# Kernel optimization log

Measured on AMD Instinct MI355X. Metric: run time of the kernel, lower is better.

Reference implementation:

```python
import jax, jax.numpy as jnp
import numpy as np

N, N1, N2, K = 65536, 16384, 8192, 16
INDIM, HID, OUT = 64, 32, 128


def _knn_np(pos, q, k, chunk=1024):
    # brute-force chunked KNN (indices into pos) for setup only
    out = []
    for s in range(0, q.shape[0], chunk):
        d = ((q[s:s + chunk, None, :] - pos[None, :, :]) ** 2).sum(-1)
        out.append(np.argpartition(d, k, axis=1)[:, :k])
    return np.concatenate(out, 0)


def setup_inputs() -> dict:
    key = jax.random.key(0)
    ks = jax.random.split(key, 12)
    x = jax.random.normal(ks[0], (N, INDIM), jnp.float32)
    pos = jax.random.uniform(ks[1], (N, 3), jnp.float32)

    pos_np = np.asarray(pos)
    rng = np.random.default_rng(0)
    idx1 = np.sort(rng.choice(N, N1, replace=False))            # RandomSampler(ratio1)
    nn1 = _knn_np(pos_np, pos_np[idx1], K)                      # [N1, K] into full cloud
    src1, dst1 = nn1.reshape(-1), np.repeat(np.arange(N1), K)
    pos1 = pos_np[idx1]
    idx2 = np.sort(rng.choice(N1, N2, replace=False))           # RandomSampler(ratio2)
    nn2 = _knn_np(pos1, pos1[idx2], K)                          # [N2, K] into level-1 cloud
    src2, dst2 = nn2.reshape(-1), np.repeat(np.arange(N2), K)

    def lin(k, i, o):
        return jax.random.normal(k, (i, o), jnp.float32) / float(np.sqrt(i))

    return dict(
        x=x, pos=pos,
        W_down=lin(ks[2], INDIM, HID), b_down=jnp.zeros((HID,), jnp.float32),
        W_pp1=lin(ks[3], 10, 32), b_pp1=jnp.zeros((32,), jnp.float32),
        W_att1=lin(ks[4], 64, 64), b_att1=jnp.zeros((64,), jnp.float32),
        W_g1=lin(ks[5], 64, 64), b_g1=jnp.zeros((64,), jnp.float32),
        W_pp2=lin(ks[6], 10, 64), b_pp2=jnp.zeros((64,), jnp.float32),
        W_att2=lin(ks[7], 128, 128), b_att2=jnp.zeros((128,), jnp.float32),
        W_g2=lin(ks[8], 128, 128), b_g2=jnp.zeros((128,), jnp.float32),
        W_up=lin(ks[9], 128, OUT), b_up=jnp.zeros((OUT,), jnp.float32),
        W_sc=lin(ks[10], INDIM, OUT), b_sc=jnp.zeros((OUT,), jnp.float32),
        idx1=jnp.asarray(idx1, jnp.int32), idx2=jnp.asarray(idx2, jnp.int32),
        src1=jnp.asarray(src1, jnp.int32), dst1=jnp.asarray(dst1, jnp.int32),
        src2=jnp.asarray(src2, jnp.int32), dst2=jnp.asarray(dst2, jnp.int32),
    )


def _mlp(h, W, b):
    return jax.nn.relu(h @ W + b)


def _randla_conv(x, pos_all, pos_q, src, dst, Wpp, bpp, Watt, batt, Wg, bg, n_out):
    # RandlaKernel.message + add-aggregate + update (bipartite: targets = sampled points)
    pos_i, pos_j = pos_q[dst], pos_all[src]                     # [E,3]
    vij = pos_i - pos_j
    dij = jnp.sqrt((vij * vij).sum(-1, keepdims=True))          # [E,1]
    rel = jnp.concatenate([pos_i, pos_j, vij, dij], axis=1)     # [E,10]
    rij = _mlp(rel, Wpp, bpp)                                   # point_pos_nn
    fij = jnp.concatenate([x[src], rij], axis=1)                # [E, c+d]
    s = jax.nn.softmax(_mlp(fij, Watt, batt), axis=-1)          # softmax over feature dim (as in source)
    agg = jax.ops.segment_sum(s * fij, dst, num_segments=n_out) # aggr='add'
    return _mlp(agg, Wg, bg)                                    # global_nn


def reference(x, pos, W_down, b_down, W_pp1, b_pp1, W_att1, b_att1, W_g1, b_g1,
              W_pp2, b_pp2, W_att2, b_att2, W_g2, b_g2, W_up, b_up, W_sc, b_sc,
              idx1, idx2, src1, dst1, src2, dst2):
    h = _mlp(x, W_down, b_down)                                 # features_downsample (indim -> outdim//4)
    pos1 = pos[idx1]
    h = _randla_conv(h, pos, pos1, src1, dst1, W_pp1, b_pp1, W_att1, b_att1, W_g1, b_g1, N1)
    pos2 = pos1[idx2]
    h = _randla_conv(h, pos1, pos2, src2, dst2, W_pp2, b_pp2, W_att2, b_att2, W_g2, b_g2, N2)
    h = _mlp(h, W_up, b_up)                                     # features_upsample
    sc = _mlp(x[idx1][idx2], W_sc, b_sc)                        # shortcut resized, idx = idx1[idx2]
    return jax.nn.relu(h + sc)
```

## Files before the change

### kernel.cpp

```cpp
#include <hip/hip_runtime.h>

#define N_FULL 65536
#define NN1    16384
#define NN2    8192

typedef __attribute__((ext_vector_type(8))) short bf16x8;
typedef __attribute__((ext_vector_type(4))) float f32x4;
typedef unsigned short ushortT;

#define MFMA16(acc, a, b) acc = __builtin_amdgcn_mfma_f32_16x16x32_bf16(a, b, acc, 0, 0, 0)

#if __has_builtin(__builtin_amdgcn_cvt_pk_bf16_f32)
typedef __attribute__((ext_vector_type(2))) __bf16 bf16x2t;
static __device__ __forceinline__ unsigned pack2(float a, float b) {
    union { bf16x2t v; unsigned u; } c;
    c.v = __builtin_amdgcn_cvt_pk_bf16_f32(a, b);
    return c.u;
}
static __device__ __forceinline__ ushortT f2bf(float f) {
    union { bf16x2t v; ushortT s[2]; } c;
    c.v = __builtin_amdgcn_cvt_pk_bf16_f32(f, 0.f);
    return c.s[0];
}
#else
static __device__ __forceinline__ ushortT f2bf(float f) {
    union { float f; unsigned u; } v; v.f = f;
    unsigned r = v.u + 0x7FFFu + ((v.u >> 16) & 1u);
    return (ushortT)(r >> 16);
}
static __device__ __forceinline__ unsigned pack2(float a, float b) {
    return (unsigned)f2bf(a) | ((unsigned)f2bf(b) << 16);
}
#endif

static __device__ __forceinline__ float bfu2f(ushortT h) {
    union { unsigned u; float f; } v; v.u = (unsigned)h << 16; return v.f;
}

#define WS_WAT1  2304
#define WS_WGT1  6912
#define WS_WAT2  11520
#define WS_WGT2  28928
#define WS_WUPT  46336
#define WS_WSCT  63744
#define WS_H0    73728
#define WS_H1    (WS_H0 + 65536u*32u)

#define SMAX_SHIFT 24.0f

static __device__ __forceinline__ void tpose(
    const float* __restrict__ src, ushortT* __restrict__ dst,
    int K, int N, int STR, int gid, int gs)
{
    for (int i = gid; i < K * N; i += gs) {
        const int n = i / K, k = i - n * K;
        dst[n * STR + k] = f2bf(src[(size_t)k * N + n]);
    }
}

__global__ __launch_bounds__(256) void k_down(
    const float* __restrict__ x, const float* __restrict__ Wd,
    const float* __restrict__ bd,
    const float* __restrict__ Wa1, const float* __restrict__ Wg1,
    const float* __restrict__ Wa2, const float* __restrict__ Wg2,
    const float* __restrict__ Wup, const float* __restrict__ Wsc,
    ushortT* __restrict__ wsw, ushortT* __restrict__ h0w)
{
    const int t = threadIdx.x;
    if (blockIdx.x >= 512) {
        const int gid = (blockIdx.x - 512) * 256 + t, gs = 68 * 256;
        tpose(Wa1, wsw + WS_WAT1, 64, 64, 72, gid, gs);
        tpose(Wg1, wsw + WS_WGT1, 64, 64, 72, gid, gs);
        tpose(Wa2, wsw + WS_WAT2, 128, 128, 136, gid, gs);
        tpose(Wg2, wsw + WS_WGT2, 128, 128, 136, gid, gs);
        tpose(Wup, wsw + WS_WUPT, 128, 128, 136, gid, gs);
        tpose(Wsc, wsw + WS_WSCT, 64, 128, 72, gid, gs);
        return;
    }

    __shared__ __align__(16) ushortT Al[128 * 72];
    __shared__ __align__(16) ushortT Bl[32 * 72];
    const int rowBase = blockIdx.x * 128;

    {
        const int r = t >> 1, c0 = (t & 1) * 32;
        unsigned* dst = (unsigned*)Al + r * 36 + (c0 >> 1);
        const float* src = &x[(size_t)(rowBase + r) * 64 + c0];
#pragma unroll
        for (int j = 0; j < 32; j += 4) {
            const float4 v = *reinterpret_cast<const float4*>(src + j);
            dst[(j >> 1) + 0] = pack2(v.x, v.y);
            dst[(j >> 1) + 1] = pack2(v.z, v.w);
        }
        const int n = t >> 3, kc = (t & 7) * 8;
        float v[8];
#pragma unroll
        for (int j = 0; j < 8; ++j) v[j] = Wd[(size_t)(kc + j) * 32 + n];
        uint4 p;
        p.x = pack2(v[0], v[1]); p.y = pack2(v[2], v[3]);
        p.z = pack2(v[4], v[5]); p.w = pack2(v[6], v[7]);
        *(uint4*)((unsigned*)Bl + n * 36 + (kc >> 1)) = p;
    }
    __syncthreads();

    const int lane = t & 63, w = t >> 6, quad = lane >> 4, c16 = lane & 15;
    f32x4 acc[2][2];
#pragma unroll
    for (int mt = 0; mt < 2; ++mt)
#pragma unroll
        for (int nt = 0; nt < 2; ++nt)
#pragma unroll
            for (int r = 0; r < 4; ++r) acc[mt][nt][r] = 0.f;
#pragma unroll
    for (int ks = 0; ks < 2; ++ks) {
        bf16x8 a[2], b[2];
#pragma unroll
        for (int mt = 0; mt < 2; ++mt)
            a[mt] = *(const bf16x8*)&Al[(w * 32 + mt * 16 + c16) * 72 + ks * 32 + quad * 8];
#pragma unroll
        for (int nt = 0; nt < 2; ++nt)
            b[nt] = *(const bf16x8*)&Bl[(nt * 16 + c16) * 72 + ks * 32 + quad * 8];
#pragma unroll
        for (int mt = 0; mt < 2; ++mt)
#pragma unroll
            for (int nt = 0; nt < 2; ++nt) MFMA16(acc[mt][nt], a[mt], b[nt]);
    }
#pragma unroll
    for (int nt = 0; nt < 2; ++nt) {
        const int col = nt * 16 + c16;
        const float bias = bd[col];
#pragma unroll
        for (int mt = 0; mt < 2; ++mt)
#pragma unroll
            for (int r = 0; r < 4; ++r) {
                const int row = rowBase + w * 32 + mt * 16 + quad * 4 + r;
                h0w[(size_t)row * 32 + col] = f2bf(fmaxf(acc[mt][nt][r] + bias, 0.f));
            }
    }
}

__global__ __launch_bounds__(256) void k_conv1(
    const ushortT* __restrict__ h0w, const float* __restrict__ pos,
    const int* __restrict__ idx1, const int* __restrict__ src1,
    const float* __restrict__ Wpp, const float* __restrict__ bpp,
    const ushortT* __restrict__ wsw, const float* __restrict__ batt,
    const float* __restrict__ bg, ushortT* __restrict__ h1w)
{
    __shared__ __align__(16) ushortT Fl[64 * 72];
    __shared__ __align__(16) ushortT A2ls[16 * 72];
    __shared__ float Pl[352];
    const int t = threadIdx.x;
    const int d0 = blockIdx.x * 4;

    for (int i = t; i < 352; i += 256) Pl[i] = (i < 320) ? Wpp[i] : bpp[i - 320];
    for (int i = t; i < 432; i += 256) ((unsigned*)A2ls)[144 + i] = 0;

    {
        const int e = t >> 2, q = t & 3;
        const int g = e >> 4;
        const int s = src1[(d0 + g) * 16 + (e & 15)];
        ((uint4*)((unsigned*)Fl + e * 36))[q] =
            ((const uint4*)((const unsigned*)h0w + (size_t)s * 16))[q];

        const int pin = idx1[d0 + g];
        const float pix = pos[pin * 3 + 0], piy = pos[pin * 3 + 1], piz = pos[pin * 3 + 2];
        const float pjx = pos[s * 3 + 0],  pjy = pos[s * 3 + 1],  pjz = pos[s * 3 + 2];
        const float vx = pix - pjx, vy = piy - pjy, vz = piz - pjz;
        const float dij = sqrtf(vx * vx + vy * vy + vz * vz);
        const float rel[10] = {pix, piy, piz, pjx, pjy, pjz, vx, vy, vz, dij};
        __syncthreads();
        const int c0 = q * 8;
#pragma unroll
        for (int c = 0; c < 8; c += 2) {
            float a0 = Pl[320 + c0 + c], a1 = Pl[320 + c0 + c + 1];
#pragma unroll
            for (int i = 0; i < 10; ++i) {
                a0 += rel[i] * Pl[i * 32 + c0 + c];
                a1 += rel[i] * Pl[i * 32 + c0 + c + 1];
            }
            ((unsigned*)Fl)[(e * 72 + 32 + c0 + c) >> 1] = pack2(fmaxf(a0, 0.f), fmaxf(a1, 0.f));
        }
    }
    __syncthreads();

    const int lane = t & 63, w = t >> 6, quad = lane >> 4, c16 = lane & 15;
    const ushortT* WB = wsw + WS_WAT1;
    f32x4 acc[4];
#pragma unroll
    for (int nt = 0; nt < 4; ++nt)
#pragma unroll
        for (int r = 0; r < 4; ++r) acc[nt][r] = 0.f;
#pragma unroll
    for (int ks = 0; ks < 2; ++ks) {
        const bf16x8 a = *(const bf16x8*)&Fl[(w * 16 + c16) * 72 + ks * 32 + quad * 8];
#pragma unroll
        for (int nt = 0; nt < 4; ++nt) {
            const bf16x8 b = *(const bf16x8*)&WB[(nt * 16 + c16) * 72 + ks * 32 + quad * 8];
            MFMA16(acc[nt], a, b);
        }
    }
    float bcol[4];
#pragma unroll
    for (int nt = 0; nt < 4; ++nt) bcol[nt] = batt[nt * 16 + c16];

    float rs[4];
#pragma unroll
    for (int r = 0; r < 4; ++r) {
        float sm = 0.f;
#pragma unroll
        for (int nt = 0; nt < 4; ++nt) {
            const float a = fmaxf(acc[nt][r] + bcol[nt], 0.f);
            acc[nt][r] = __expf(a - SMAX_SHIFT);
            sm += acc[nt][r];
        }
        sm += __shfl_xor(sm, 1);
        sm += __shfl_xor(sm, 2);
        sm += __shfl_xor(sm, 4);
        sm += __shfl_xor(sm, 8);
        rs[r] = 1.f / sm;
    }
#pragma unroll
    for (int nt = 0; nt < 4; ++nt) {
        float v = 0.f;
#pragma unroll
        for (int r = 0; r < 4; ++r) {
            const float fv = bfu2f(Fl[(w * 16 + quad * 4 + r) * 72 + nt * 16 + c16]);
            v += acc[nt][r] * rs[r] * fv;
        }
        v += __shfl_xor(v, 16);
        v += __shfl_xor(v, 32);
        if (lane < 16)
            A2ls[w * 72 + nt * 16 + c16] = f2bf(v);
    }
    __syncthreads();

    {
        const ushortT* GB = wsw + WS_WGT1;
        f32x4 acc2 = {0.f, 0.f, 0.f, 0.f};
#pragma unroll
        for (int ks = 0; ks < 2; ++ks) {
            const bf16x8 a = *(const bf16x8*)&A2ls[c16 * 72 + ks * 32 + quad * 8];
            const bf16x8 b = *(const bf16x8*)&GB[(w * 16 + c16) * 72 + ks * 32 + quad * 8];
            MFMA16(acc2, a, b);
        }
        const int col = w * 16 + c16;
        const float bias = bg[col];
        if (quad == 0) {
#pragma unroll
            for (int r = 0; r < 4; ++r)
                h1w[(size_t)(d0 + r) * 64 + col] = f2bf(fmaxf(acc2[r] + bias, 0.f));
        }
    }
}

__global__ __launch_bounds__(256) void k_conv2f(
    const ushortT* __restrict__ h1w, const float* __restrict__ pos,
    const float* __restrict__ x,
    const int* __restrict__ idx1, const int* __restrict__ idx2,
    const int* __restrict__ src2,
    const float* __restrict__ Wpp, const float* __restrict__ bpp,
    const ushortT* __restrict__ wsw, const float* __restrict__ batt,
    const float* __restrict__ bg, const float* __restrict__ bup,
    const float* __restrict__ bsc, float* __restrict__ out)
{
    __shared__ __align__(16) ushortT Fl[64 * 136];
    __shared__ __align__(16) ushortT AGG[16 * 136];
    __shared__ __align__(16) ushortT H2[16 * 136];
    __shared__ float Pl[704];
    const int t = threadIdx.x;
    const int d0 = blockIdx.x * 4;

    for (int i = t; i < 704; i += 256) Pl[i] = (i < 640) ? Wpp[i] : bpp[i - 640];
    for (int i = t; i < 816; i += 256) ((unsigned*)AGG)[272 + i] = 0;

    {
        const int e = t >> 2, q = t & 3;
        const int g = e >> 4;
        const int s = src2[(d0 + g) * 16 + (e & 15)];
        {
            const uint4* srcp = (const uint4*)((const unsigned*)h1w + (size_t)s * 32);
            uint4* dstp = (uint4*)((unsigned*)Fl + e * 68);
            dstp[q * 2 + 0] = srcp[q * 2 + 0];
            dstp[q * 2 + 1] = srcp[q * 2 + 1];
        }
        const int pin = idx1[idx2[d0 + g]];
        const int sn = idx1[s];
        const float pix = pos[pin * 3 + 0], piy = pos[pin * 3 + 1], piz = pos[pin * 3 + 2];
        const float pjx = pos[sn * 3 + 0],  pjy = pos[sn * 3 + 1],  pjz = pos[sn * 3 + 2];
        const float vx = pix - pjx, vy = piy - pjy, vz = piz - pjz;
        const float dij = sqrtf(vx * vx + vy * vy + vz * vz);
        const float rel[10] = {pix, piy, piz, pjx, pjy, pjz, vx, vy, vz, dij};
        __syncthreads();
        const int c0 = q * 16;
#pragma unroll
        for (int c = 0; c < 16; c += 2) {
            float a0 = Pl[640 + c0 + c], a1 = Pl[640 + c0 + c + 1];
#pragma unroll
            for (int i = 0; i < 10; ++i) {
                a0 += rel[i] * Pl[i * 64 + c0 + c];
                a1 += rel[i] * Pl[i * 64 + c0 + c + 1];
            }
            ((unsigned*)Fl)[(e * 136 + 64 + c0 + c) >> 1] = pack2(fmaxf(a0, 0.f), fmaxf(a1, 0.f));
        }
    }
    __syncthreads();

    const int lane = t & 63, w = t >> 6, quad = lane >> 4, c16 = lane & 15;
    const ushortT* WB = wsw + WS_WAT2;
    f32x4 acc[8];
#pragma unroll
    for (int nt = 0; nt < 8; ++nt)
#pragma unroll
        for (int r = 0; r < 4; ++r) acc[nt][r] = 0.f;
#pragma unroll
    for (int ks = 0; ks < 4; ++ks) {
        const bf16x8 a = *(const bf16x8*)&Fl[(w * 16 + c16) * 136 + ks * 32 + quad * 8];
#pragma unroll
        for (int nt = 0; nt < 8; ++nt) {
            const bf16x8 b = *(const bf16x8*)&WB[(nt * 16 + c16) * 136 + ks * 32 + quad * 8];
            MFMA16(acc[nt], a, b);
        }
    }
    float bcol[8];
#pragma unroll
    for (int nt = 0; nt < 8; ++nt) bcol[nt] = batt[nt * 16 + c16];

    float rs[4];
#pragma unroll
    for (int r = 0; r < 4; ++r) {
        float sm = 0.f;
#pragma unroll
        for (int nt = 0; nt < 8; ++nt) {
            const float a = fmaxf(acc[nt][r] + bcol[nt], 0.f);
            acc[nt][r] = __expf(a - SMAX_SHIFT);
            sm += acc[nt][r];
        }
        sm += __shfl_xor(sm, 1);
        sm += __shfl_xor(sm, 2);
        sm += __shfl_xor(sm, 4);
        sm += __shfl_xor(sm, 8);
        rs[r] = 1.f / sm;
    }
#pragma unroll
    for (int nt = 0; nt < 8; ++nt) {
        float v = 0.f;
#pragma unroll
        for (int r = 0; r < 4; ++r) {
            const float fv = bfu2f(Fl[(w * 16 + quad * 4 + r) * 136 + nt * 16 + c16]);
            v += acc[nt][r] * rs[r] * fv;
        }
        v += __shfl_xor(v, 16);
        v += __shfl_xor(v, 32);
        if (lane < 16)
            AGG[w * 136 + nt * 16 + c16] = f2bf(v);
    }
    __syncthreads();


    {
        const ushortT* GB = wsw + WS_WGT2;
        f32x4 g[2];
#pragma unroll
        for (int j = 0; j < 2; ++j)
#pragma unroll
            for (int r = 0; r < 4; ++r) g[j][r] = 0.f;
#pragma unroll
        for (int ks = 0; ks < 4; ++ks) {
            const bf16x8 a = *(const bf16x8*)&AGG[c16 * 136 + ks * 32 + quad * 8];
#pragma unroll
            for (int j = 0; j < 2; ++j) {
                const bf16x8 b = *(const bf16x8*)&GB[((w * 2 + j) * 16 + c16) * 136 + ks * 32 + quad * 8];
                MFMA16(g[j], a, b);
            }
        }
#pragma unroll
        for (int j = 0; j < 2; ++j) {
            const int col = (w * 2 + j) * 16 + c16;
            const float bias = bg[col];
#pragma unroll
            for (int r = 0; r < 4; ++r)
                H2[(quad * 4 + r) * 136 + col] = f2bf(fmaxf(g[j][r] + bias, 0.f));
        }
    }
    __syncthreads();

    f32x4 u[2];
    {
        const ushortT* UB = wsw + WS_WUPT;
#pragma unroll
        for (int j = 0; j < 2; ++j)
#pragma unroll
            for (int r = 0; r < 4; ++r) u[j][r] = 0.f;
#pragma unroll
        for (int ks = 0; ks < 4; ++ks) {
            const bf16x8 a = *(const bf16x8*)&H2[c16 * 136 + ks * 32 + quad * 8];
#pragma unroll
            for (int j = 0; j < 2; ++j) {
                const bf16x8 b = *(const bf16x8*)&UB[((w * 2 + j) * 16 + c16) * 136 + ks * 32 + quad * 8];
                MFMA16(u[j], a, b);
            }
        }
#pragma unroll
        for (int j = 0; j < 2; ++j) {
            const float bias = bup[(w * 2 + j) * 16 + c16];
#pragma unroll
            for (int r = 0; r < 4; ++r) u[j][r] = fmaxf(u[j][r] + bias, 0.f);
        }
    }

    {
        const ushortT* SB = wsw + WS_WSCT;
        const int pinx = idx1[idx2[d0 + (c16 & 3)]];
        const float* xrow = &x[(size_t)pinx * 64];
        f32x4 s[2];
#pragma unroll
        for (int j = 0; j < 2; ++j)
#pragma unroll
            for (int r = 0; r < 4; ++r) s[j][r] = 0.f;
#pragma unroll
        for (int ks = 0; ks < 2; ++ks) {
            const float4 v0 = *reinterpret_cast<const float4*>(xrow + ks * 32 + quad * 8);
            const float4 v1 = *reinterpret_cast<const float4*>(xrow + ks * 32 + quad * 8 + 4);
            union { bf16x8 v; unsigned u[4]; } a;
            a.u[0] = pack2(v0.x, v0.y); a.u[1] = pack2(v0.z, v0.w);
            a.u[2] = pack2(v1.x, v1.y); a.u[3] = pack2(v1.z, v1.w);
#pragma unroll
            for (int j = 0; j < 2; ++j) {
                const bf16x8 b = *(const bf16x8*)&SB[((w * 2 + j) * 16 + c16) * 72 + ks * 32 + quad * 8];
                MFMA16(s[j], a.v, b);
            }
        }
        if (quad == 0) {
#pragma unroll
            for (int j = 0; j < 2; ++j) {
                const int col = (w * 2 + j) * 16 + c16;
                const float bias = bsc[col];
#pragma unroll
                for (int r = 0; r < 4; ++r) {
                    const float sc = fmaxf(s[j][r] + bias, 0.f);
                    out[(size_t)(d0 + r) * 128 + col] = u[j][r] + sc;
                }
            }
        }
    }
}

extern "C" void kernel_launch(void* const* d_in, const int* in_sizes, int n_in,
                              void* d_out, int out_size, void* d_ws, size_t ws_size,
                              hipStream_t stream)
{
    const float* x      = (const float*)d_in[0];
    const float* pos    = (const float*)d_in[1];
    const float* W_down = (const float*)d_in[2];
    const float* b_down = (const float*)d_in[3];
    const float* W_pp1  = (const float*)d_in[4];
    const float* b_pp1  = (const float*)d_in[5];
    const float* W_att1 = (const float*)d_in[6];
    const float* b_att1 = (const float*)d_in[7];
    const float* W_g1   = (const float*)d_in[8];
    const float* b_g1   = (const float*)d_in[9];
    const float* W_pp2  = (const float*)d_in[10];
    const float* b_pp2  = (const float*)d_in[11];
    const float* W_att2 = (const float*)d_in[12];
    const float* b_att2 = (const float*)d_in[13];
    const float* W_g2   = (const float*)d_in[14];
    const float* b_g2   = (const float*)d_in[15];
    const float* W_up   = (const float*)d_in[16];
    const float* b_up   = (const float*)d_in[17];
    const float* W_sc   = (const float*)d_in[18];
    const float* b_sc   = (const float*)d_in[19];
    const int* idx1 = (const int*)d_in[20];
    const int* idx2 = (const int*)d_in[21];
    const int* src1 = (const int*)d_in[22];
    const int* src2 = (const int*)d_in[24];

    ushortT* wsw = (ushortT*)d_ws;
    ushortT* h0w = wsw + WS_H0;
    ushortT* h1w = wsw + WS_H1;

    k_down  <<<512 + 68, 256, 0, stream>>>(x, W_down, b_down,
                                           W_att1, W_g1, W_att2, W_g2, W_up, W_sc,
                                           wsw, h0w);
    k_conv1 <<<NN1 / 4, 256, 0, stream>>>(h0w, pos, idx1, src1,
                                          W_pp1, b_pp1, wsw, b_att1, b_g1, h1w);
    k_conv2f<<<NN2 / 4, 256, 0, stream>>>(h1w, pos, x, idx1, idx2, src2,
                                          W_pp2, b_pp2, wsw, b_att2,
                                          b_g2, b_up, b_sc, (float*)d_out);
}
```

Before: 180.4 us.

## Process eight destination points per block to fill MFMA rows in conv kernels

New measurement: 170.9 us (median of 2 runs). 1.06x faster.

```diff
diff --git a/kernel.cpp b/kernel.cpp
--- a/kernel.cpp
+++ b/kernel.cpp
@@ -139,21 +139,21 @@
     }
 }
 
-__global__ __launch_bounds__(256) void k_conv1(
+__global__ __launch_bounds__(512) void k_conv1(
     const ushortT* __restrict__ h0w, const float* __restrict__ pos,
     const int* __restrict__ idx1, const int* __restrict__ src1,
     const float* __restrict__ Wpp, const float* __restrict__ bpp,
     const ushortT* __restrict__ wsw, const float* __restrict__ batt,
     const float* __restrict__ bg, ushortT* __restrict__ h1w)
 {
-    __shared__ __align__(16) ushortT Fl[64 * 72];
+    __shared__ __align__(16) ushortT Fl[128 * 72];
     __shared__ __align__(16) ushortT A2ls[16 * 72];
     __shared__ float Pl[352];
     const int t = threadIdx.x;
-    const int d0 = blockIdx.x * 4;
-
-    for (int i = t; i < 352; i += 256) Pl[i] = (i < 320) ? Wpp[i] : bpp[i - 320];
-    for (int i = t; i < 432; i += 256) ((unsigned*)A2ls)[144 + i] = 0;
+    const int d0 = blockIdx.x * 8;
+
+    for (int i = t; i < 352; i += 512) Pl[i] = (i < 320) ? Wpp[i] : bpp[i - 320];
+    for (int i = t; i < 288; i += 512) ((unsigned*)A2ls)[288 + i] = 0;
 
     {
         const int e = t >> 2, q = t & 3;
@@ -234,7 +234,7 @@
     }
     __syncthreads();
 
-    {
+    if (w < 4) {
         const ushortT* GB = wsw + WS_WGT1;
         f32x4 acc2 = {0.f, 0.f, 0.f, 0.f};
 #pragma unroll
@@ -245,15 +245,17 @@
         }
         const int col = w * 16 + c16;
         const float bias = bg[col];
-        if (quad == 0) {
-#pragma unroll
-            for (int r = 0; r < 4; ++r)
-                h1w[(size_t)(d0 + r) * 64 + col] = f2bf(fmaxf(acc2[r] + bias, 0.f));
-        }
-    }
-}
-
-__global__ __launch_bounds__(256) void k_conv2f(
+        if (quad < 2) {
+#pragma unroll
+            for (int r = 0; r < 4; ++r) {
+                const int row = quad * 4 + r;
+                h1w[(size_t)(d0 + row) * 64 + col] = f2bf(fmaxf(acc2[r] + bias, 0.f));
+            }
+        }
+    }
+}
+
+__global__ __launch_bounds__(512) void k_conv2f(
     const ushortT* __restrict__ h1w, const float* __restrict__ pos,
     const float* __restrict__ x,
     const int* __restrict__ idx1, const int* __restrict__ idx2,
@@ -263,15 +265,15 @@
     const float* __restrict__ bg, const float* __restrict__ bup,
     const float* __restrict__ bsc, float* __restrict__ out)
 {
-    __shared__ __align__(16) ushortT Fl[64 * 136];
+    __shared__ __align__(16) ushortT Fl[128 * 136];
     __shared__ __align__(16) ushortT AGG[16 * 136];
     __shared__ __align__(16) ushortT H2[16 * 136];
     __shared__ float Pl[704];
     const int t = threadIdx.x;
-    const int d0 = blockIdx.x * 4;
-
-    for (int i = t; i < 704; i += 256) Pl[i] = (i < 640) ? Wpp[i] : bpp[i - 640];
-    for (int i = t; i < 816; i += 256) ((unsigned*)AGG)[272 + i] = 0;
+    const int d0 = blockIdx.x * 8;
+
+    for (int i = t; i < 704; i += 512) Pl[i] = (i < 640) ? Wpp[i] : bpp[i - 640];
+    for (int i = t; i < 544; i += 512) ((unsigned*)AGG)[544 + i] = 0;
 
     {
         const int e = t >> 2, q = t & 3;
@@ -359,64 +361,40 @@
 
     {
         const ushortT* GB = wsw + WS_WGT2;
-        f32x4 g[2];
-#pragma unroll
-        for (int j = 0; j < 2; ++j)
-#pragma unroll
-            for (int r = 0; r < 4; ++r) g[j][r] = 0.f;
+        f32x4 g = {0.f, 0.f, 0.f, 0.f};
 #pragma unroll
         for (int ks = 0; ks < 4; ++ks) {
             const bf16x8 a = *(const bf16x8*)&AGG[c16 * 136 + ks * 32 + quad * 8];
-#pragma unroll
-            for (int j = 0; j < 2; ++j) {
-                const bf16x8 b = *(const bf16x8*)&GB[((w * 2 + j) * 16 + c16) * 136 + ks * 32 + quad * 8];
-                MFMA16(g[j], a, b);
-            }
-        }
-#pragma unroll
-        for (int j = 0; j < 2; ++j) {
-            const int col = (w * 2 + j) * 16 + c16;
-            const float bias = bg[col];
-#pragma unroll
-            for (int r = 0; r < 4; ++r)
-                H2[(quad * 4 + r) * 136 + col] = f2bf(fmaxf(g[j][r] + bias, 0.f));
-        }
-    }
-    __syncthreads();
-
-    f32x4 u[2];
+            const bf16x8 b = *(const bf16x8*)&GB[(w * 16 + c16) * 136 + ks * 32 + quad * 8];
+            MFMA16(g, a, b);
+        }
+        const int col = w * 16 + c16;
+        const float bias = bg[col];
+#pragma unroll
+        for (int r = 0; r < 4; ++r)
+            H2[(quad * 4 + r) * 136 + col] = f2bf(fmaxf(g[r] + bias, 0.f));
+    }
+    __syncthreads();
+
+    f32x4 u = {0.f, 0.f, 0.f, 0.f};
     {
         const ushortT* UB = wsw + WS_WUPT;
-#pragma unroll
-        for (int j = 0; j < 2; ++j)
-#pragma unroll
-            for (int r = 0; r < 4; ++r) u[j][r] = 0.f;
 #pragma unroll
         for (int ks = 0; ks < 4; ++ks) {
             const bf16x8 a = *(const bf16x8*)&H2[c16 * 136 + ks * 32 + quad * 8];
-#pragma unroll
-            for (int j = 0; j < 2; ++j) {
-                const bf16x8 b = *(const bf16x8*)&UB[((w * 2 + j) * 16 + c16) * 136 + ks * 32 + quad * 8];
-                MFMA16(u[j], a, b);
-            }
-        }
-#pragma unroll
-        for (int j = 0; j < 2; ++j) {
-            const float bias = bup[(w * 2 + j) * 16 + c16];
-#pragma unroll
-            for (int r = 0; r < 4; ++r) u[j][r] = fmaxf(u[j][r] + bias, 0.f);
-        }
+            const bf16x8 b = *(const bf16x8*)&UB[(w * 16 + c16) * 136 + ks * 32 + quad * 8];
+            MFMA16(u, a, b);
+        }
+        const float bias = bup[w * 16 + c16];
+#pragma unroll
+        for (int r = 0; r < 4; ++r) u[r] = fmaxf(u[r] + bias, 0.f);
     }
 
     {
         const ushortT* SB = wsw + WS_WSCT;
-        const int pinx = idx1[idx2[d0 + (c16 & 3)]];
+        const int pinx = idx1[idx2[d0 + (c16 & 7)]];
         const float* xrow = &x[(size_t)pinx * 64];
-        f32x4 s[2];
-#pragma unroll
-        for (int j = 0; j < 2; ++j)
-#pragma unroll
-            for (int r = 0; r < 4; ++r) s[j][r] = 0.f;
+        f32x4 s = {0.f, 0.f, 0.f, 0.f};
 #pragma unroll
         for (int ks = 0; ks < 2; ++ks) {
             const float4 v0 = *reinterpret_cast<const float4*>(xrow + ks * 32 + quad * 8);
@@ -424,22 +402,16 @@
             union { bf16x8 v; unsigned u[4]; } a;
             a.u[0] = pack2(v0.x, v0.y); a.u[1] = pack2(v0.z, v0.w);
             a.u[2] = pack2(v1.x, v1.y); a.u[3] = pack2(v1.z, v1.w);
-#pragma unroll
-            for (int j = 0; j < 2; ++j) {
-                const bf16x8 b = *(const bf16x8*)&SB[((w * 2 + j) * 16 + c16) * 72 + ks * 32 + quad * 8];
-                MFMA16(s[j], a.v, b);
-            }
-        }
-        if (quad == 0) {
-#pragma unroll
-            for (int j = 0; j < 2; ++j) {
-                const int col = (w * 2 + j) * 16 + c16;
-                const float bias = bsc[col];
-#pragma unroll
-                for (int r = 0; r < 4; ++r) {
-                    const float sc = fmaxf(s[j][r] + bias, 0.f);
-                    out[(size_t)(d0 + r) * 128 + col] = u[j][r] + sc;
-                }
+            const bf16x8 b = *(const bf16x8*)&SB[(w * 16 + c16) * 72 + ks * 32 + quad * 8];
+            MFMA16(s, a.v, b);
+        }
+        if (quad < 2) {
+            const int col = w * 16 + c16;
+            const float bias = bsc[col];
+#pragma unroll
+            for (int r = 0; r < 4; ++r) {
+                const float sc = fmaxf(s[r] + bias, 0.f);
+                out[(size_t)(d0 + quad * 4 + r) * 128 + col] = u[r] + sc;
             }
         }
     }
@@ -481,9 +453,9 @@
     k_down  <<<512 + 68, 256, 0, stream>>>(x, W_down, b_down,
                                            W_att1, W_g1, W_att2, W_g2, W_up, W_sc,
                                            wsw, h0w);
-    k_conv1 <<<NN1 / 4, 256, 0, stream>>>(h0w, pos, idx1, src1,
+    k_conv1 <<<NN1 / 8, 512, 0, stream>>>(h0w, pos, idx1, src1,
                                           W_pp1, b_pp1, wsw, b_att1, b_g1, h1w);
-    k_conv2f<<<NN2 / 4, 256, 0, stream>>>(h1w, pos, x, idx1, idx2, src2,
+    k_conv2f<<<NN2 / 8, 512, 0, stream>>>(h1w, pos, x, idx1, idx2, src2,
                                           W_pp2, b_pp2, wsw, b_att2,
                                           b_g2, b_up, b_sc, (float*)d_out);
 }
```
